# Kernel tuning notes

Hardware: AMD Instinct MI355X
Metric: run time of the kernel (lower is better)

## Reference

```python
import jax, jax.numpy as jnp
import numpy as np

N = 100000  # num nodes
E = 1600000  # num edges


def gcn_conv(x, edge_index, W, b):
    """PyG-style GCNConv: add self-loops, symmetric deg^-1/2 normalization,
    message = norm * (x @ W) gathered from src, scatter-add to dst, then + bias."""
    n = x.shape[0]
    loop = jnp.arange(n)
    src = jnp.concatenate([edge_index[0], loop])
    dst = jnp.concatenate([edge_index[1], loop])
    deg = jax.ops.segment_sum(jnp.ones_like(dst, dtype=x.dtype), dst, num_segments=n)
    dinv = jnp.where(deg > 0, jax.lax.rsqrt(deg), jnp.zeros_like(deg))
    norm = dinv[src] * dinv[dst]  # [E+N]
    h = x @ W  # dense transform first (out_dim <= in_dim here)
    msg = h[src] * norm[:, None]  # gather + scale, [E+N, out]
    out = jax.ops.segment_sum(msg, dst, num_segments=n)  # scatter-add
    return out + b


def setup_inputs() -> dict:
    key = jax.random.key(0)
    ks = jax.random.split(key, 6)
    x = jax.random.normal(ks[0], (N, 165), dtype=jnp.float32)
    edge_index = jax.random.randint(ks[1], (2, E), 0, N, dtype=jnp.int64)
    W1 = jax.random.normal(ks[2], (165, 128), dtype=jnp.float32) * 0.05
    b1 = jnp.zeros((128,), dtype=jnp.float32)
    W2 = jax.random.normal(ks[3], (128, 2), dtype=jnp.float32) * 0.05
    b2 = jnp.zeros((2,), dtype=jnp.float32)
    Ws = jax.random.normal(ks[4], (165, 2), dtype=jnp.float32) * 0.05
    bs = jnp.zeros((2,), dtype=jnp.float32)
    return {"x": x, "edge_index": edge_index, "W1": W1, "b1": b1,
            "W2": W2, "b2": b2, "Ws": Ws, "bs": bs}


def reference(x, edge_index, W1, b1, W2, b2, Ws, bs):
    h = jax.nn.relu(gcn_conv(x, edge_index, W1, b1))
    # dropout is identity at inference (training=False)
    out = gcn_conv(h, edge_index, W2, b2)
    return out + (x @ Ws + bs)
```

## Files before the change

kernel.cpp:

```cpp
#include <hip/hip_runtime.h>
#include <hip/hip_bf16.h>


#define IND 165
#define HID 128
#define KP 192
#define BM 32
#define XSS2 208
#define SLAB 8192
#define MAXNB 512

typedef __attribute__((ext_vector_type(8))) short short8v;
typedef __attribute__((ext_vector_type(4))) float float4v;
typedef __attribute__((ext_vector_type(2))) float float2v;

__device__ __forceinline__ unsigned short f2bf(float f) {
    unsigned u = __float_as_uint(f);
    unsigned r = (u + 0x7FFF + ((u >> 16) & 1)) >> 16;
    return (unsigned short)r;
}
__device__ __forceinline__ float bf2f(unsigned short s) { return __uint_as_float(((unsigned)s) << 16); }

__global__ __launch_bounds__(256) void setup_kernel(const float* __restrict__ W1,
                                                    unsigned short* __restrict__ w1t,
                                                    const int* __restrict__ e32,
                                                    int* __restrict__ flag,
                                                    int* __restrict__ bucket_len, int NB) {
    int b = blockIdx.x;
    if (b < 96) {
        int t = b * 256 + threadIdx.x;
        int nn = t / KP, k = t - nn * KP;
        w1t[t] = (k < IND) ? f2bf(W1[k * HID + nn]) : (unsigned short)0;
    } else {
        __shared__ int nz;
        if (threadIdx.x == 0) nz = 0;
        __syncthreads();
        if (e32[2 * threadIdx.x + 1] != 0) atomicOr(&nz, 1);
        __syncthreads();
        if (threadIdx.x == 0) flag[0] = (nz == 0) ? 1 : 0;
        for (int t = threadIdx.x; t < NB; t += 256) bucket_len[t] = 0;
    }
}

__global__ __launch_bounds__(256) void partition_kernel(const int* __restrict__ e32,
                                                        const int* __restrict__ flag,
                                                        int* __restrict__ bucket_len,
                                                        unsigned* __restrict__ slab,
                                                        int E, int NB) {
    __shared__ unsigned hist[MAXNB];
    __shared__ unsigned runbase[MAXNB];
    __shared__ unsigned cnt2[MAXNB];
    for (int t = threadIdx.x; t < NB; t += 256) { hist[t] = 0; cnt2[t] = 0; }
    __syncthreads();
    const int f = flag[0];
    const int base = blockIdx.x * 8192;
    unsigned rec[32];
    unsigned bk[32];
    #pragma unroll
    for (int j = 0; j < 32; ++j) {
        int e = base + j * 256 + threadIdx.x;
        if (e < E) {
            int src, dst;
            if (f) {
                int2 s2 = ((const int2*)e32)[e];
                int2 d2 = ((const int2*)e32)[E + e];
                src = s2.x; dst = d2.x;
            } else {
                src = e32[e];
                dst = e32[E + e];
            }
            unsigned b = (unsigned)dst >> 8;
            rec[j] = ((unsigned)(dst & 255) << 24) | (unsigned)src;
            bk[j] = b;
            atomicAdd(&hist[b], 1u);
        } else {
            bk[j] = 0xFFFFFFFFu;
            rec[j] = 0;
        }
    }
    __syncthreads();
    for (int t = threadIdx.x; t < NB; t += 256) {
        unsigned h = hist[t];
        runbase[t] = h ? (unsigned)atomicAdd(&bucket_len[t], (int)h) : 0u;
    }
    __syncthreads();
    #pragma unroll
    for (int j = 0; j < 32; ++j) {
        unsigned b = bk[j];
        if (b != 0xFFFFFFFFu) {
            unsigned p = runbase[b] + atomicAdd(&cnt2[b], 1u);
            if (p < SLAB) slab[(size_t)b * SLAB + p] = rec[j];
        }
    }
}

__global__ __launch_bounds__(256) void buildb_kernel(const unsigned* __restrict__ slab,
                                                     const int* __restrict__ bucket_len,
                                                     int2* __restrict__ row2,
                                                     float* __restrict__ dinv,
                                                     int* __restrict__ col_src, int n) {
    __shared__ unsigned deg[256];
    __shared__ int qa[256], qb[256];
    __shared__ unsigned cur[256];
    const int b = blockIdx.x;
    const int t = threadIdx.x;
    const int len = min(bucket_len[b], SLAB);
    const unsigned* recs = slab + (size_t)b * SLAB;
    const int d0 = b << 8;
    const int base = b * SLAB;
    deg[t] = 0;
    __syncthreads();
    for (int i = t; i < len; i += 256) atomicAdd(&deg[recs[i] >> 24], 1u);
    __syncthreads();
    const unsigned dv = deg[t];
    const int pdv = (int)((dv + 7u) & ~7u);
    qa[t] = pdv;
    __syncthreads();
    int* s = qa; int* d = qb;
    for (int off = 1; off < 256; off <<= 1) {
        d[t] = s[t] + ((t >= off) ? s[t - off] : 0);
        __syncthreads();
        int* tmp = s; s = d; d = tmp;
    }
    int pexcl = s[t] - pdv;
    int pend = min(pexcl + pdv, SLAB);
    if (pexcl > SLAB) pexcl = SLAB;
    if (d0 + t < n) {
        dinv[d0 + t] = rsqrtf(1.0f + (float)dv);
        row2[d0 + t] = make_int2(base + pexcl, base + pend);
    }
    cur[t] = (unsigned)pexcl;
    __syncthreads();
    for (int i = t; i < len; i += 256) {
        unsigned r = recs[i];
        unsigned p = atomicAdd(&cur[r >> 24], 1u);
        if (p < (unsigned)SLAB) col_src[base + p] = (int)(r & 0xFFFFFFu);
    }
    for (int p = pexcl + (int)dv; p < pend; ++p)
        col_src[base + p] = n;
}

__global__ __launch_bounds__(256, 4) void gemm1_kernel(const float* __restrict__ x,
                                                       const unsigned short* __restrict__ w1t,
                                                       const float* __restrict__ Ws,
                                                       const float* __restrict__ bs,
                                                       const float* __restrict__ b2,
                                                       const float* __restrict__ dinv,
                                                       unsigned char* __restrict__ hb8,
                                                       float* __restrict__ h2p,
                                                       float* __restrict__ skip, int n) {
    __shared__ unsigned short xs[BM * XSS2];
    __shared__ float sdinv[BM];
    const int row0 = blockIdx.x * BM;
    const int tid = threadIdx.x;
    const int wave = tid >> 6, lane = tid & 63;
    const int l15 = lane & 15, lk = (lane >> 4) * 8;

    if (blockIdx.x == 0) {
        if (tid < 32) ((unsigned*)(hb8 + (size_t)n * HID))[tid] = 0u;
        if (tid == 32) ((float2*)h2p)[n] = make_float2(0.f, 0.f);
    }
    if (tid < BM) sdinv[tid] = (row0 + tid < n) ? dinv[row0 + tid] : 1.f;

    short8v bfr[12];
    #pragma unroll
    for (int nt2 = 0; nt2 < 2; ++nt2)
        #pragma unroll
        for (int ks = 0; ks < 6; ++ks)
            bfr[nt2 * 6 + ks] =
                *(const short8v*)(w1t + (size_t)((2 * wave + nt2) * 16 + l15) * KP + ks * 32 + lk);

    for (int t = tid; t < BM * (XSS2 - IND); t += 256) {
        int r = t / (XSS2 - IND), k = IND + (t - r * (XSS2 - IND));
        xs[r * XSS2 + k] = 0;
    }
    {
        const int rows = min(BM, n - row0);
        const int nflt = rows * IND;
        const float2* xsrc = (const float2*)(x + (size_t)row0 * IND);
        const int nf2 = nflt >> 1;
        for (int f = tid; f < nf2; f += 256) {
            float2 v = xsrc[f];
            int e0 = 2 * f;
            int r0 = e0 / IND, k0 = e0 - r0 * IND;
            xs[r0 * XSS2 + k0] = f2bf(v.x);
            int r1 = (k0 == IND - 1) ? r0 + 1 : r0;
            int k1 = (k0 == IND - 1) ? 0 : k0 + 1;
            xs[r1 * XSS2 + k1] = f2bf(v.y);
        }
        if ((nflt & 1) && tid == 0) {
            int e = nflt - 1;
            int r = e / IND, k = e - r * IND;
            xs[r * XSS2 + k] = f2bf(x[(size_t)row0 * IND + e]);
        }
    }
    __syncthreads();

    float4v acc[2][2];
    #pragma unroll
    for (int m = 0; m < 2; ++m)
        #pragma unroll
        for (int nt2 = 0; nt2 < 2; ++nt2) acc[m][nt2] = (float4v){0.f, 0.f, 0.f, 0.f};
    #pragma unroll
    for (int m = 0; m < 2; ++m) {
        const unsigned short* arow = xs + (m * 16 + l15) * XSS2;
        #pragma unroll
        for (int ks = 0; ks < 6; ++ks) {
            short8v a = *(const short8v*)(arow + ks * 32 + lk);
            acc[m][0] = __builtin_amdgcn_mfma_f32_16x16x32_bf16(a, bfr[ks], acc[m][0], 0, 0, 0);
            acc[m][1] = __builtin_amdgcn_mfma_f32_16x16x32_bf16(a, bfr[6 + ks], acc[m][1], 0, 0, 0);
        }
    }

    #pragma unroll
    for (int m = 0; m < 2; ++m) {
        int rib0 = m * 16 + (lane >> 4) * 4;
        #pragma unroll
        for (int nt2 = 0; nt2 < 2; ++nt2) {
            int col = (2 * wave + nt2) * 16 + l15;
            #pragma unroll
            for (int r = 0; r < 4; ++r) {
                int row = row0 + rib0 + r;
                float hv = acc[m][nt2][r] * sdinv[rib0 + r];
                int pk = __builtin_amdgcn_cvt_pk_fp8_f32(hv, 0.f, 0, false);
                if (row < n) hb8[(size_t)row * HID + col] = (unsigned char)(pk & 0xFF);
            }
        }
    }

    {
        int r = tid >> 3, j = tid & 7;
        int row = row0 + r;
        float s0 = 0.f, s1 = 0.f;
        if (row < n) {
            const float2* Wsv = (const float2*)Ws;
            const unsigned short* xr = xs + r * XSS2;
            for (int k = j; k < IND; k += 8) {
                float xv = bf2f(xr[k]);
                float2 w = Wsv[k];
                s0 = fmaf(xv, w.x, s0);
                s1 = fmaf(xv, w.y, s1);
            }
        }
        s0 += __shfl_xor(s0, 1); s0 += __shfl_xor(s0, 2); s0 += __shfl_xor(s0, 4);
        s1 += __shfl_xor(s1, 1); s1 += __shfl_xor(s1, 2); s1 += __shfl_xor(s1, 4);
        if (j == 0 && row < n)
            ((float2*)skip)[row] = make_float2(s0 + bs[0] + b2[0], s1 + bs[1] + b2[1]);
    }
}

__global__ __launch_bounds__(256) void agg1_kernel(const unsigned char* __restrict__ hb8,
                                                   const float* __restrict__ dinv,
                                                   const int2* __restrict__ row2,
                                                   const int* __restrict__ col_src,
                                                   const float* __restrict__ b1,
                                                   const float* __restrict__ W2,
                                                   float* __restrict__ h2p, int n) {
    int wid = threadIdx.x >> 6, lane = threadIdx.x & 63;
    int i = blockIdx.x * 4 + wid;
    if (i >= n) return;
    const int slot = lane >> 4, cl = lane & 15;
    const float di = dinv[i];
    float2v a0, a1, a2, a3;
    {
        uint2 r = *(const uint2*)(hb8 + (size_t)i * 128 + cl * 8);
        float w = (slot == 0) ? 1.f : 0.f;
        float2v wv = {w, w};
        a0 = __builtin_amdgcn_cvt_pk_f32_fp8((int)r.x, false) * wv;
        a1 = __builtin_amdgcn_cvt_pk_f32_fp8((int)r.x, true)  * wv;
        a2 = __builtin_amdgcn_cvt_pk_f32_fp8((int)r.y, false) * wv;
        a3 = __builtin_amdgcn_cvt_pk_f32_fp8((int)r.y, true)  * wv;
    }
    const int2 be = row2[i];
    const int beg  = __builtin_amdgcn_readfirstlane(be.x);
    const int endv = __builtin_amdgcn_readfirstlane(be.y);
    for (int e = beg; e < endv; e += 8) {
        int4 c0 = *(const int4*)(col_src + e);
        int4 c1 = *(const int4*)(col_src + e + 4);
        int sx0 = (slot & 1) ? c0.y : c0.x;
        int sy0 = (slot & 1) ? c0.w : c0.z;
        int s0  = (slot & 2) ? sy0 : sx0;
        int sx1 = (slot & 1) ? c1.y : c1.x;
        int sy1 = (slot & 1) ? c1.w : c1.z;
        int s1  = (slot & 2) ? sy1 : sx1;
        uint2 r0 = *(const uint2*)(hb8 + (size_t)s0 * 128 + cl * 8);
        uint2 r1 = *(const uint2*)(hb8 + (size_t)s1 * 128 + cl * 8);
        a0 += __builtin_amdgcn_cvt_pk_f32_fp8((int)r0.x, false);
        a1 += __builtin_amdgcn_cvt_pk_f32_fp8((int)r0.x, true);
        a2 += __builtin_amdgcn_cvt_pk_f32_fp8((int)r0.y, false);
        a3 += __builtin_amdgcn_cvt_pk_f32_fp8((int)r0.y, true);
        a0 += __builtin_amdgcn_cvt_pk_f32_fp8((int)r1.x, false);
        a1 += __builtin_amdgcn_cvt_pk_f32_fp8((int)r1.x, true);
        a2 += __builtin_amdgcn_cvt_pk_f32_fp8((int)r1.y, false);
        a3 += __builtin_amdgcn_cvt_pk_f32_fp8((int)r1.y, true);
    }
    float a[8] = {a0.x, a0.y, a1.x, a1.y, a2.x, a2.y, a3.x, a3.y};
    #pragma unroll
    for (int c = 0; c < 8; ++c) {
        a[c] += __shfl_xor(a[c], 16);
        a[c] += __shfl_xor(a[c], 32);
    }
    float4 bA = ((const float4*)b1)[2 * cl];
    float4 bB = ((const float4*)b1)[2 * cl + 1];
    float v0 = fmaxf(fmaf(di, a[0], bA.x), 0.f);
    float v1 = fmaxf(fmaf(di, a[1], bA.y), 0.f);
    float v2 = fmaxf(fmaf(di, a[2], bA.z), 0.f);
    float v3 = fmaxf(fmaf(di, a[3], bA.w), 0.f);
    float v4 = fmaxf(fmaf(di, a[4], bB.x), 0.f);
    float v5 = fmaxf(fmaf(di, a[5], bB.y), 0.f);
    float v6 = fmaxf(fmaf(di, a[6], bB.z), 0.f);
    float v7 = fmaxf(fmaf(di, a[7], bB.w), 0.f);
    float4 wA = ((const float4*)W2)[4 * cl];
    float4 wB = ((const float4*)W2)[4 * cl + 1];
    float4 wC = ((const float4*)W2)[4 * cl + 2];
    float4 wD = ((const float4*)W2)[4 * cl + 3];
    float p0 = v0 * wA.x + v1 * wA.z + v2 * wB.x + v3 * wB.z
             + v4 * wC.x + v5 * wC.z + v6 * wD.x + v7 * wD.z;
    float p1 = v0 * wA.y + v1 * wA.w + v2 * wB.y + v3 * wB.w
             + v4 * wC.y + v5 * wC.w + v6 * wD.y + v7 * wD.w;
    p0 += __shfl_xor(p0, 1); p0 += __shfl_xor(p0, 2);
    p0 += __shfl_xor(p0, 4); p0 += __shfl_xor(p0, 8);
    p1 += __shfl_xor(p1, 1); p1 += __shfl_xor(p1, 2);
    p1 += __shfl_xor(p1, 4); p1 += __shfl_xor(p1, 8);
    if (lane == 0) ((float2*)h2p)[i] = make_float2(p0 * di, p1 * di);
}

__global__ __launch_bounds__(256) void agg2_kernel(const float* __restrict__ h2p,
                                                   const float* __restrict__ dinv,
                                                   const int2* __restrict__ row2,
                                                   const int* __restrict__ col_src,
                                                   const float* __restrict__ skip,
                                                   float* __restrict__ out, int n) {
    int wid = threadIdx.x >> 6, lane = threadIdx.x & 63;
    int i = blockIdx.x * 4 + wid;
    if (i >= n) return;
    float di = dinv[i];
    float a0 = 0.f, a1 = 0.f;
    const int2 be = row2[i];
    const int beg  = __builtin_amdgcn_readfirstlane(be.x);
    const int endv = __builtin_amdgcn_readfirstlane(be.y);
    for (int e = beg + lane; e < endv; e += 64) {
        int s = col_src[e];
        float2 hs = ((const float2*)h2p)[s];
        a0 += hs.x;
        a1 += hs.y;
    }
    #pragma unroll
    for (int off = 32; off; off >>= 1) {
        a0 += __shfl_xor(a0, off);
        a1 += __shfl_xor(a1, off);
    }
    if (lane == 0) {
        float2 self = ((const float2*)h2p)[i];
        float2 sk = ((const float2*)skip)[i];
        ((float2*)out)[i] = make_float2(di * (a0 + self.x) + sk.x,
                                        di * (a1 + self.y) + sk.y);
    }
}

extern "C" void kernel_launch(void* const* d_in, const int* in_sizes, int n_in,
                              void* d_out, int out_size, void* d_ws, size_t ws_size,
                              hipStream_t stream) {
    const float* x  = (const float*)d_in[0];
    const int*   ei = (const int*)d_in[1];
    const float* W1 = (const float*)d_in[2];
    const float* b1 = (const float*)d_in[3];
    const float* W2 = (const float*)d_in[4];
    const float* b2 = (const float*)d_in[5];
    const float* Ws = (const float*)d_in[6];
    const float* bs = (const float*)d_in[7];
    float* out = (float*)d_out;

    const int n = in_sizes[0] / IND;
    const int E = in_sizes[1] / 2;
    const int NB = (n + 255) >> 8;

    char* ws = (char*)d_ws;
    size_t off = 0;
    auto alloc = [&](size_t bytes) { void* p = ws + off; off += (bytes + 255) & ~(size_t)255; return p; };
    int*            flag        = (int*)alloc(256);
    int*            bucket_len  = (int*)alloc((size_t)(MAXNB + 1) * 4);
    unsigned*       slab        = (unsigned*)alloc((size_t)NB * SLAB * 4);
    int2*           row2        = (int2*)alloc((size_t)n * 8);
    float*          dinv        = (float*)alloc((size_t)n * 4);
    int*            col_src     = (int*)alloc((size_t)NB * SLAB * 4);
    unsigned char*  hb8         = (unsigned char*)alloc((size_t)(n + 1) * HID);
    float*          h2p         = (float*)alloc((size_t)(n + 1) * 2 * 4);
    float*          skip        = (float*)alloc((size_t)n * 2 * 4);
    unsigned short* w1t         = (unsigned short*)alloc((size_t)HID * KP * 2);
    (void)ws_size;

    setup_kernel<<<97, 256, 0, stream>>>(W1, w1t, ei, flag, bucket_len, NB);
    partition_kernel<<<(E + 8191) / 8192, 256, 0, stream>>>(ei, flag, bucket_len, slab, E, NB);
    buildb_kernel<<<NB, 256, 0, stream>>>(slab, bucket_len, row2, dinv, col_src, n);

    gemm1_kernel<<<(n + BM - 1) / BM, 256, 0, stream>>>(x, w1t, Ws, bs, b2, dinv, hb8, h2p, skip, n);
    agg1_kernel<<<(n + 3) / 4, 256, 0, stream>>>(hb8, dinv, row2, col_src, b1, W2, h2p, n);
    agg2_kernel<<<(n + 3) / 4, 256, 0, stream>>>(h2p, dinv, row2, col_src, skip, out, n);
}
```

Before: 167.5 us.

## Use 16-lane groups per node in agg2, batch x loads, cache Ws in LDS

```diff
diff --git a/kernel.cpp b/kernel.cpp
--- a/kernel.cpp
+++ b/kernel.cpp
@@ -151,6 +151,7 @@
                                                        float* __restrict__ skip, int n) {
     __shared__ unsigned short xs[BM * XSS2];
     __shared__ float sdinv[BM];
+    __shared__ float2 wss[IND];
     const int row0 = blockIdx.x * BM;
     const int tid = threadIdx.x;
     const int wave = tid >> 6, lane = tid & 63;
@@ -161,6 +162,7 @@
         if (tid == 32) ((float2*)h2p)[n] = make_float2(0.f, 0.f);
     }
     if (tid < BM) sdinv[tid] = (row0 + tid < n) ? dinv[row0 + tid] : 1.f;
+    if (tid < IND) wss[tid] = ((const float2*)Ws)[tid];
 
     short8v bfr[12];
     #pragma unroll
@@ -176,22 +178,39 @@
     }
     {
         const int rows = min(BM, n - row0);
-        const int nflt = rows * IND;
         const float2* xsrc = (const float2*)(x + (size_t)row0 * IND);
-        const int nf2 = nflt >> 1;
-        for (int f = tid; f < nf2; f += 256) {
-            float2 v = xsrc[f];
-            int e0 = 2 * f;
-            int r0 = e0 / IND, k0 = e0 - r0 * IND;
-            xs[r0 * XSS2 + k0] = f2bf(v.x);
-            int r1 = (k0 == IND - 1) ? r0 + 1 : r0;
-            int k1 = (k0 == IND - 1) ? 0 : k0 + 1;
-            xs[r1 * XSS2 + k1] = f2bf(v.y);
-        }
-        if ((nflt & 1) && tid == 0) {
-            int e = nflt - 1;
-            int r = e / IND, k = e - r * IND;
-            xs[r * XSS2 + k] = f2bf(x[(size_t)row0 * IND + e]);
+        if (rows == BM) {
+            float2 v[11];
+            #pragma unroll
+            for (int j = 0; j < 10; ++j) v[j] = xsrc[j * 256 + tid];
+            if (tid < 80) v[10] = xsrc[2560 + tid];
+            #pragma unroll
+            for (int j = 0; j < 11; ++j) {
+                if (j == 10 && tid >= 80) break;
+                int e0 = 2 * (j * 256 + tid);
+                int r0 = e0 / IND, k0 = e0 - r0 * IND;
+                xs[r0 * XSS2 + k0] = f2bf(v[j].x);
+                int r1 = (k0 == IND - 1) ? r0 + 1 : r0;
+                int k1 = (k0 == IND - 1) ? 0 : k0 + 1;
+                xs[r1 * XSS2 + k1] = f2bf(v[j].y);
+            }
+        } else {
+            const int nflt = rows * IND;
+            const int nf2 = nflt >> 1;
+            for (int f = tid; f < nf2; f += 256) {
+                float2 v = xsrc[f];
+                int e0 = 2 * f;
+                int r0 = e0 / IND, k0 = e0 - r0 * IND;
+                xs[r0 * XSS2 + k0] = f2bf(v.x);
+                int r1 = (k0 == IND - 1) ? r0 + 1 : r0;
+                int k1 = (k0 == IND - 1) ? 0 : k0 + 1;
+                xs[r1 * XSS2 + k1] = f2bf(v.y);
+            }
+            if ((nflt & 1) && tid == 0) {
+                int e = nflt - 1;
+                int r = e / IND, k = e - r * IND;
+                xs[r * XSS2 + k] = f2bf(x[(size_t)row0 * IND + e]);
+            }
         }
     }
     __syncthreads();
@@ -233,11 +252,10 @@
         int row = row0 + r;
         float s0 = 0.f, s1 = 0.f;
         if (row < n) {
-            const float2* Wsv = (const float2*)Ws;
             const unsigned short* xr = xs + r * XSS2;
             for (int k = j; k < IND; k += 8) {
                 float xv = bf2f(xr[k]);
-                float2 w = Wsv[k];
+                float2 w = wss[k];
                 s0 = fmaf(xv, w.x, s0);
                 s1 = fmaf(xv, w.y, s1);
             }
@@ -331,26 +349,25 @@
                                                    const int* __restrict__ col_src,
                                                    const float* __restrict__ skip,
                                                    float* __restrict__ out, int n) {
-    int wid = threadIdx.x >> 6, lane = threadIdx.x & 63;
-    int i = blockIdx.x * 4 + wid;
+    const int tid = threadIdx.x;
+    const int grp = tid >> 4;
+    const int el  = tid & 15;
+    const int i = blockIdx.x * 16 + grp;
     if (i >= n) return;
-    float di = dinv[i];
+    const float di = dinv[i];
+    const int2 be = row2[i];
     float a0 = 0.f, a1 = 0.f;
-    const int2 be = row2[i];
-    const int beg  = __builtin_amdgcn_readfirstlane(be.x);
-    const int endv = __builtin_amdgcn_readfirstlane(be.y);
-    for (int e = beg + lane; e < endv; e += 64) {
+    for (int e = be.x + el; e < be.y; e += 16) {
         int s = col_src[e];
         float2 hs = ((const float2*)h2p)[s];
         a0 += hs.x;
         a1 += hs.y;
     }
-    #pragma unroll
-    for (int off = 32; off; off >>= 1) {
-        a0 += __shfl_xor(a0, off);
-        a1 += __shfl_xor(a1, off);
-    }
-    if (lane == 0) {
+    a0 += __shfl_xor(a0, 1); a0 += __shfl_xor(a0, 2);
+    a0 += __shfl_xor(a0, 4); a0 += __shfl_xor(a0, 8);
+    a1 += __shfl_xor(a1, 1); a1 += __shfl_xor(a1, 2);
+    a1 += __shfl_xor(a1, 4); a1 += __shfl_xor(a1, 8);
+    if (el == 0) {
         float2 self = ((const float2*)h2p)[i];
         float2 sk = ((const float2*)skip)[i];
         ((float2*)out)[i] = make_float2(di * (a0 + self.x) + sk.x,
@@ -396,5 +413,5 @@
 
     gemm1_kernel<<<(n + BM - 1) / BM, 256, 0, stream>>>(x, w1t, Ws, bs, b2, dinv, hb8, h2p, skip, n);
     agg1_kernel<<<(n + 3) / 4, 256, 0, stream>>>(hb8, dinv, row2, col_src, b1, W2, h2p, n);
-    agg2_kernel<<<(n + 3) / 4, 256, 0, stream>>>(h2p, dinv, row2, col_src, skip, out, n);
-}
+    agg2_kernel<<<(n + 15) / 16, 256, 0, stream>>>(h2p, dinv, row2, col_src, skip, out, n);
+}
```

Measured after the change: 146.2 us. 1.15x faster.
